# Optimization experiments

Measured on AMD Instinct MI355X. Metric: run time of the kernel, lower is better.

The kernel has to match this reference:

```python
import jax, jax.numpy as jnp
import numpy as np

S = 2048
HIDDEN = 4096
NH, NKV, HD = 32, 8, 128
QPK = NH // NKV  # 4
BLOCK, LOCAL, VERT = 64, 16, 8
ROPE_BASE = 1.0e6
SCALE = 1.0 / HD  # mup scaling: head_dim / mup_attn_multiplier(=1.0)


def setup_inputs() -> dict:
    key = jax.random.key(0)
    ks = jax.random.split(key, 5)
    qkv_out = NKV * (QPK + 2) * HD  # 6144, head-major layout
    return {
        "positions": jnp.arange(S, dtype=jnp.int32),
        "hidden_states": jax.random.normal(ks[0], (S, HIDDEN), jnp.float32),
        "w_qkv": jax.random.normal(ks[1], (qkv_out, HIDDEN), jnp.float32) * 0.02,
        "b_qkv": jax.random.normal(ks[2], (qkv_out,), jnp.float32) * 0.02,
        "w_dense": jax.random.normal(ks[3], (HIDDEN, HIDDEN), jnp.float32) * 0.02,
        "b_dense": jax.random.normal(ks[4], (HIDDEN,), jnp.float32) * 0.02,
    }


def _rope(x, cos, sin):
    # NeoX-style (non-interleaved) rotary over full head_dim.
    # x: [S, n_heads, HD]; cos/sin: [S, HD//2]
    d2 = x.shape[-1] // 2
    x1, x2 = x[..., :d2], x[..., d2:]
    c, s = cos[:, None, :], sin[:, None, :]
    return jnp.concatenate([x1 * c - x2 * s, x2 * c + x1 * s], axis=-1)


def _blocksparse_mask(positions):
    # vllm phi3small pattern: block (qb,kb) active iff causal AND
    # (qb-kb < local_blocks OR (kb + head + 1) % vert_stride == 0), hetero heads.
    qb = positions // BLOCK                       # [S]
    heads = jnp.arange(NH, dtype=positions.dtype)
    diff = qb[:, None] - qb[None, :]              # [S,S]
    local = diff < LOCAL                          # [S,S]
    vert = ((qb[None, None, :] + heads[:, None, None] + 1) % VERT) == 0  # [NH,1,S]
    causal = positions[:, None] >= positions[None, :]                     # [S,S]
    return (local[None] | vert) & causal[None]    # [NH,S,S]


def reference(positions, hidden_states, w_qkv, b_qkv, w_dense, b_dense):
    seq = hidden_states.shape[0]
    qkv = hidden_states @ w_qkv.T + b_qkv                   # [S, 6144]
    qkv = qkv.reshape(seq, NKV, QPK + 2, HD)                # head-major split
    q = qkv[:, :, :QPK].reshape(seq, NH, HD)
    k = qkv[:, :, QPK]                                      # [S, NKV, HD]
    v = qkv[:, :, QPK + 1]

    pos = positions.astype(jnp.float32)  # rope_position_scale = 1.0
    inv_freq = 1.0 / (ROPE_BASE ** (jnp.arange(0, HD, 2, dtype=jnp.float32) / HD))
    freqs = pos[:, None] * inv_freq                          # [S, HD/2]
    cos, sin = jnp.cos(freqs), jnp.sin(freqs)
    q = _rope(q, cos, sin)
    k = _rope(k, cos, sin)

    # GQA: each kv head serves QPK query heads
    kx = jnp.repeat(k, QPK, axis=1)                          # [S, NH, HD]
    vx = jnp.repeat(v, QPK, axis=1)

    scores = jnp.einsum('qhd,khd->hqk', q, kx) * SCALE       # [NH,S,S]
    mask = _blocksparse_mask(positions)
    scores = jnp.where(mask, scores, -jnp.inf)  # diag always in local block -> no empty rows
    p = jax.nn.softmax(scores, axis=-1)
    out = jnp.einsum('hqk,khd->qhd', p, vx).reshape(seq, NH * HD)
    return out @ w_dense.T + b_dense
```

## Files before the change

kernel.cpp:

```cpp
#include <hip/hip_runtime.h>

#define S_LEN   2048
#define HID     4096
#define NHEADS  32
#define NKVH    8
#define HDIM    128
#define NQKV    6144
#define ATT_SCALE (1.0f/128.0f)

typedef unsigned short u16;
typedef __attribute__((ext_vector_type(8))) __bf16 bf16x8;
typedef __attribute__((ext_vector_type(4))) float  f32x4;

__device__ __forceinline__ u16 f2bf(float f) {
    union { float f; unsigned u; } x; x.f = f;
    unsigned u = x.u;
    u += 0x7fffu + ((u >> 16) & 1u);
    return (u16)(u >> 16);
}
__device__ __forceinline__ float bf2f(u16 v) {
    union { unsigned u; float f; } x; x.u = ((unsigned)v) << 16; return x.f;
}

__global__ __launch_bounds__(256) void cvt_bf16_kernel(const float* __restrict__ in,
                                                       u16* __restrict__ out, int n4) {
    int stride = gridDim.x * blockDim.x;
    for (int i = blockIdx.x * blockDim.x + threadIdx.x; i < n4; i += stride) {
        float4 v = *(const float4*)(in + (size_t)i * 4);
        ushort4 o = make_ushort4(f2bf(v.x), f2bf(v.y), f2bf(v.z), f2bf(v.w));
        *(ushort4*)(out + (size_t)i * 4) = o;
    }
}

#define BM 128
#define BN 128
#define BK 32

template <bool OUT_BF16>
__global__ __launch_bounds__(256) void gemm_bt_kernel(
    const u16* __restrict__ A,
    const u16* __restrict__ B,
    const float* __restrict__ bias,
    void* __restrict__ Cout,
    int M, int N, int K)
{
    __shared__ u16 Alds[2][BM][BK];
    __shared__ u16 Blds[2][BN][BK];

    const int tid  = threadIdx.x;
    const int wid  = tid >> 6;
    const int lane = tid & 63;
    const int ln   = lane & 15;
    const int quad = lane >> 4;
    const int wm   = (wid >> 1) * 64;
    const int wn   = (wid & 1) * 64;
    const int tileM = blockIdx.y * BM;
    const int tileN = blockIdx.x * BN;

    const int srow = lane >> 2;
    const int scol = ((lane & 3) ^ ((srow >> 1) & 3)) * 8;

    f32x4 acc[4][4];
    #pragma unroll
    for (int i = 0; i < 4; i++)
        #pragma unroll
        for (int j = 0; j < 4; j++) {
            f32x4 z = {0.f, 0.f, 0.f, 0.f};
            acc[i][j] = z;
        }

    auto stage = [&](int k, int buf) {
        const int k0 = k * BK;
        #pragma unroll
        for (int p = 0; p < 2; p++) {
            int r = p * 64 + wid * 16;
            const u16* ga = A + (size_t)(tileM + r + srow) * K + k0 + scol;
            const u16* gb = B + (size_t)(tileN + r + srow) * K + k0 + scol;
            __builtin_amdgcn_global_load_lds(
                (const __attribute__((address_space(1))) void*)ga,
                (__attribute__((address_space(3))) void*)&Alds[buf][r][0], 16, 0, 0);
            __builtin_amdgcn_global_load_lds(
                (const __attribute__((address_space(1))) void*)gb,
                (__attribute__((address_space(3))) void*)&Blds[buf][r][0], 16, 0, 0);
        }
    };

    const int nIter = K / BK;
    stage(0, 0);

    const int pc = (quad ^ ((ln >> 1) & 3)) * 8;

    for (int k = 0; k < nIter; k++) {
        const int buf = k & 1;
        __syncthreads();
        if (k + 1 < nIter) stage(k + 1, buf ^ 1);

        bf16x8 af[4], bfr[4];
        #pragma unroll
        for (int i = 0; i < 4; i++)
            af[i] = *(const bf16x8*)(&Alds[buf][wm + i * 16 + ln][pc]);
        #pragma unroll
        for (int j = 0; j < 4; j++)
            bfr[j] = *(const bf16x8*)(&Blds[buf][wn + j * 16 + ln][pc]);
        #pragma unroll
        for (int i = 0; i < 4; i++)
            #pragma unroll
            for (int j = 0; j < 4; j++)
                acc[i][j] = __builtin_amdgcn_mfma_f32_16x16x32_bf16(af[i], bfr[j], acc[i][j], 0, 0, 0);
    }

    #pragma unroll
    for (int i = 0; i < 4; i++) {
        #pragma unroll
        for (int j = 0; j < 4; j++) {
            int n = tileN + wn + j * 16 + ln;
            float bv = bias[n];
            #pragma unroll
            for (int r = 0; r < 4; r++) {
                int m = tileM + wm + i * 16 + quad * 4 + r;
                float v = acc[i][j][r] + bv;
                if (OUT_BF16)
                    ((u16*)Cout)[(size_t)m * N + n] = f2bf(v);
                else
                    ((float*)Cout)[(size_t)m * N + n] = v;
            }
        }
    }
}

#define TBM 256
#define TBN 256
#define TBK 64

#define GFENCE() asm volatile("" ::: "memory")
#define GSBAR()  do { GFENCE(); __builtin_amdgcn_s_barrier(); GFENCE(); } while (0)

template <bool OUT_BF16>
__global__ __launch_bounds__(512, 2) void gemm_bt8_kernel(
    const u16* __restrict__ A,
    const u16* __restrict__ B,
    const float* __restrict__ bias,
    void* __restrict__ Cout,
    int M, int N, int K)
{
    __shared__ u16 lds[65536];

    const int tid  = threadIdx.x;
    const int wid  = tid >> 6;
    const int lane = tid & 63;
    const int ln   = lane & 15;
    const int quad = lane >> 4;
    const int wr   = wid >> 2;
    const int wc   = wid & 3;
    const int tileM = blockIdx.y * TBM;
    const int tileN = blockIdx.x * TBN;

    f32x4 acc[2][2][4][2];
    #pragma unroll
    for (int a = 0; a < 2; a++)
        #pragma unroll
        for (int b = 0; b < 2; b++)
            #pragma unroll
            for (int m = 0; m < 4; m++)
                #pragma unroll
                for (int n = 0; n < 2; n++) {
                    f32x4 z = {0.f, 0.f, 0.f, 0.f};
                    acc[a][b][m][n] = z;
                }

    const int srho = lane >> 3;
    const int scol = (((lane & 7) ^ srho) << 3);

    auto stage_half = [&](const u16* Mp, int tbase, int h, int kk, int bb, int isB) {
        const int ldsbase = isB * 32768 + (bb * 2 + h) * 8192;
        #pragma unroll
        for (int s = 0; s < 2; s++) {
            const int rho0 = s * 64 + wid * 8;
            const int rho  = rho0 + srho;
            const u16* src = Mp + (size_t)(tbase + h * 128 + rho) * K + (size_t)kk * TBK + scol;
            __builtin_amdgcn_global_load_lds(
                (const __attribute__((address_space(1))) void*)src,
                (__attribute__((address_space(3))) void*)&lds[ldsbase + rho0 * 64], 16, 0, 0);
        }
    };

    bf16x8 af[4][2];

#define READ_A(a_)                                                                  \
    do {                                                                            \
        _Pragma("unroll")                                                           \
        for (int m = 0; m < 4; m++) {                                               \
            const int ra = wr * 64 + m * 16 + ln;                                   \
            const int ab = (buf * 2 + (a_)) * 8192 + ra * 64;                       \
            const int rx = ra & 7;                                                  \
            af[m][0] = *(const bf16x8*)(&lds[ab + ((quad ^ rx) << 3)]);             \
            af[m][1] = *(const bf16x8*)(&lds[ab + (((4 + quad) ^ rx) << 3)]);       \
        }                                                                           \
    } while (0)

#define READ_B(b_, bfr_)                                                            \
    do {                                                                            \
        _Pragma("unroll")                                                           \
        for (int n = 0; n < 2; n++) {                                               \
            const int rb = wc * 32 + n * 16 + ln;                                   \
            const int bbase = 32768 + (buf * 2 + (b_)) * 8192 + rb * 64;            \
            const int rx = rb & 7;                                                  \
            bfr_[n][0] = *(const bf16x8*)(&lds[bbase + ((quad ^ rx) << 3)]);        \
            bfr_[n][1] = *(const bf16x8*)(&lds[bbase + (((4 + quad) ^ rx) << 3)]);  \
        }                                                                           \
    } while (0)

#define DO_MFMA(a_, b_, bfr_)                                                       \
    do {                                                                            \
        __builtin_amdgcn_s_setprio(1);                                              \
        _Pragma("unroll")                                                           \
        for (int m = 0; m < 4; m++)                                                 \
            _Pragma("unroll")                                                       \
            for (int n = 0; n < 2; n++) {                                           \
                acc[a_][b_][m][n] = __builtin_amdgcn_mfma_f32_16x16x32_bf16(        \
                    af[m][0], bfr_[n][0], acc[a_][b_][m][n], 0, 0, 0);              \
                acc[a_][b_][m][n] = __builtin_amdgcn_mfma_f32_16x16x32_bf16(        \
                    af[m][1], bfr_[n][1], acc[a_][b_][m][n], 0, 0, 0);              \
            }                                                                       \
        __builtin_amdgcn_s_setprio(0);                                              \
    } while (0)

    const int nIter = K / TBK;

    stage_half(A, tileM, 0, 0, 0, 0);
    stage_half(B, tileN, 0, 0, 0, 1);
    stage_half(A, tileM, 1, 0, 0, 0);
    stage_half(B, tileN, 1, 0, 0, 1);

    for (int t = 0; t < nIter; t++) {
        const int buf = t & 1;
        const int bn  = buf ^ 1;
        const int kn  = (t + 1 == nIter) ? 0 : t + 1;

        stage_half(A, tileM, 0, kn, bn, 0);
        asm volatile("s_waitcnt vmcnt(6)" ::: "memory");
        GSBAR();
        {
            bf16x8 bfr[2][2];
            READ_A(0); READ_B(0, bfr);
            DO_MFMA(0, 0, bfr);
            GSBAR();

            stage_half(B, tileN, 0, kn, bn, 1);
            asm volatile("s_waitcnt vmcnt(4)" ::: "memory");
            GSBAR();
            READ_A(1);
            DO_MFMA(1, 0, bfr);
            GSBAR();
        }

        stage_half(A, tileM, 1, kn, bn, 0);
        GSBAR();
        {
            bf16x8 bfr[2][2];
            READ_B(1, bfr);
            DO_MFMA(1, 1, bfr);
            GSBAR();

            stage_half(B, tileN, 1, kn, bn, 1);
            GSBAR();
            READ_A(0);
            DO_MFMA(0, 1, bfr);
            GSBAR();
        }
    }

    asm volatile("s_waitcnt vmcnt(0)" ::: "memory");

#undef READ_A
#undef READ_B
#undef DO_MFMA

    #pragma unroll
    for (int a = 0; a < 2; a++)
        #pragma unroll
        for (int b = 0; b < 2; b++)
            #pragma unroll
            for (int n = 0; n < 2; n++) {
                #pragma unroll
                for (int m = 0; m < 4; m++) {
                    const int col = tileN + b * 128 + wc * 32 + n * 16 + ln;
                    const float bv = bias[col];
                    #pragma unroll
                    for (int r = 0; r < 4; r++) {
                        const int row = tileM + a * 128 + wr * 64 + m * 16 + quad * 4 + r;
                        float v = acc[a][b][m][n][r] + bv;
                        if (OUT_BF16)
                            ((u16*)Cout)[(size_t)row * N + col] = f2bf(v);
                        else
                            ((float*)Cout)[(size_t)row * N + col] = v;
                    }
                }
            }
}

__global__ __launch_bounds__(128) void rope_split_kernel(
    const u16* __restrict__ qkv, const int* __restrict__ positions,
    u16* __restrict__ qb_o, u16* __restrict__ kb_o, u16* __restrict__ vb_o)
{
    const int d   = threadIdx.x;
    const int pos = blockIdx.x;
    const int hy  = blockIdx.y;
    const float p = (float)positions[pos];

    if (hy >= NHEADS + NKVH) {
        int kv = hy - NHEADS - NKVH;
        const u16* src = qkv + (size_t)pos * NQKV + (kv * 6 + 5) * HDIM;
        vb_o[((size_t)kv * S_LEN + pos) * HDIM + d] = src[d];
        return;
    }
    const u16* src;
    u16* dst;
    if (hy < NHEADS) {
        int kv = hy >> 2, qi = hy & 3;
        src = qkv + (size_t)pos * NQKV + (kv * 6 + qi) * HDIM;
        dst = qb_o + ((size_t)hy * S_LEN + pos) * HDIM;
    } else {
        int kv = hy - NHEADS;
        src = qkv + (size_t)pos * NQKV + (kv * 6 + 4) * HDIM;
        dst = kb_o + ((size_t)kv * S_LEN + pos) * HDIM;
    }
    int d2 = d & 63;
    float inv = expf(-(float)d2 * (13.815510557964274f / 64.0f));
    float fr = p * inv;
    float s, c;
    sincosf(fr, &s, &c);
    float x1 = bf2f(src[d2]);
    float x2 = bf2f(src[d2 + 64]);
    float o = (d < 64) ? (x1 * c - x2 * s) : (x2 * c + x1 * s);
    dst[d] = f2bf(o);
}

__global__ __launch_bounds__(256, 4) void attn_bs_kernel(
    const u16* __restrict__ Q,
    const u16* __restrict__ K,
    const u16* __restrict__ V,
    u16* __restrict__ O)
{
    __shared__ u16 Ks[64 * 128];
    __shared__ u16 Vt[128 * 64];
    __shared__ u16 Ps[4][16 * 64];

    const int qb = (int)gridDim.x - 1 - (int)blockIdx.x;
    const int h  = blockIdx.y;
    const int kv = h >> 2;
    const int tid  = threadIdx.x;
    const int w    = tid >> 6;
    const int lane = tid & 63;
    const int ln   = lane & 15;
    const int quad = lane >> 4;

    bf16x8 aq[4];
    {
        const u16* Qg = Q + ((size_t)h * S_LEN + qb * 64 + w * 16 + ln) * HDIM + quad * 8;
        #pragma unroll
        for (int ks = 0; ks < 4; ks++)
            aq[ks] = *(const bf16x8*)(Qg + ks * 32);
    }

    f32x4 oacc[8];
    #pragma unroll
    for (int n = 0; n < 8; n++) { f32x4 z = {0.f,0.f,0.f,0.f}; oacc[n] = z; }
    float mrow[4] = {-1e30f, -1e30f, -1e30f, -1e30f};
    float lrow[4] = {0.f, 0.f, 0.f, 0.f};

    for (int kb = 0; kb <= qb; kb++) {
        bool sel = (qb - kb < 16) || (((kb + h + 1) & 7) == 0);
        if (!sel) continue;

        __syncthreads();

        const u16* Kg = K + ((size_t)kv * S_LEN + kb * 64) * HDIM;
        const u16* Vg = V + ((size_t)kv * S_LEN + kb * 64) * HDIM;

        #pragma unroll
        for (int p = 0; p < 4; p++) {
            int r0  = w * 16 + p * 4;
            int row = r0 + (lane >> 4);
            const u16* src = Kg + (size_t)row * HDIM + (((lane & 15) ^ (row & 7)) << 3);
            __builtin_amdgcn_global_load_lds(
                (const __attribute__((address_space(1))) void*)src,
                (__attribute__((address_space(3))) void*)&Ks[r0 * 128], 16, 0, 0);
        }

        {
            int dbase = w * 32;
            #pragma unroll
            for (int p = 0; p < 4; p++) {
                int d0 = dbase + p * 8;
                uint4 vv = *(const uint4*)(Vg + (size_t)lane * HDIM + d0);
                const u16* pvv = (const u16*)&vv;
                #pragma unroll
                for (int jj = 0; jj < 8; jj++) {
                    int d = d0 + jj;
                    Vt[d * 64 + ((((lane >> 3)) ^ (d & 7)) << 3) + (lane & 7)] = pvv[jj];
                }
            }
        }
        __syncthreads();

        f32x4 sacc[4];
        #pragma unroll
        for (int jj = 0; jj < 4; jj++) { f32x4 z = {0.f,0.f,0.f,0.f}; sacc[jj] = z; }
        __builtin_amdgcn_s_setprio(1);
        #pragma unroll
        for (int ks = 0; ks < 4; ks++) {
            #pragma unroll
            for (int jj = 0; jj < 4; jj++) {
                bf16x8 bk = *(const bf16x8*)(
                    &Ks[(jj * 16 + ln) * 128 + (((ks * 4 + quad) ^ (ln & 7)) << 3)]);
                sacc[jj] = __builtin_amdgcn_mfma_f32_16x16x32_bf16(aq[ks], bk, sacc[jj], 0, 0, 0);
            }
        }
        __builtin_amdgcn_s_setprio(0);

        #pragma unroll
        for (int r = 0; r < 4; r++) {
            float pv[4];
            float mx = -1e30f;
            const int qrow = w * 16 + quad * 4 + r;
            #pragma unroll
            for (int jj = 0; jj < 4; jj++) {
                float s = sacc[jj][r] * ATT_SCALE;
                if (kb == qb && (jj * 16 + ln) > qrow) s = -1e30f;
                pv[jj] = s;
                mx = fmaxf(mx, s);
            }
            #pragma unroll
            for (int off = 1; off < 16; off <<= 1)
                mx = fmaxf(mx, __shfl_xor(mx, off, 64));
            float mnew  = fmaxf(mrow[r], mx);
            float alpha = __expf(mrow[r] - mnew);
            float sum = 0.f;
            #pragma unroll
            for (int jj = 0; jj < 4; jj++) {
                float pe = __expf(pv[jj] - mnew);
                pv[jj] = pe;
                sum += pe;
            }
            #pragma unroll
            for (int off = 1; off < 16; off <<= 1)
                sum += __shfl_xor(sum, off, 64);
            lrow[r] = lrow[r] * alpha + sum;
            mrow[r] = mnew;
            #pragma unroll
            for (int n = 0; n < 8; n++) oacc[n][r] *= alpha;
            const int prow = quad * 4 + r;
            #pragma unroll
            for (int jj = 0; jj < 4; jj++)
                Ps[w][prow * 64 + (((jj * 2 + (ln >> 3)) ^ (prow & 7)) << 3) + (ln & 7)]
                    = f2bf(pv[jj]);
        }

        __builtin_amdgcn_s_setprio(1);
        #pragma unroll
        for (int kk = 0; kk < 2; kk++) {
            bf16x8 ap = *(const bf16x8*)(
                &Ps[w][ln * 64 + (((kk * 4 + quad) ^ (ln & 7)) << 3)]);
            #pragma unroll
            for (int n = 0; n < 8; n++) {
                bf16x8 bv = *(const bf16x8*)(
                    &Vt[(n * 16 + ln) * 64 + (((kk * 4 + quad) ^ (ln & 7)) << 3)]);
                oacc[n] = __builtin_amdgcn_mfma_f32_16x16x32_bf16(ap, bv, oacc[n], 0, 0, 0);
            }
        }
        __builtin_amdgcn_s_setprio(0);
    }

    #pragma unroll
    for (int n = 0; n < 8; n++) {
        #pragma unroll
        for (int r = 0; r < 4; r++) {
            int row = w * 16 + quad * 4 + r;
            int pos = qb * 64 + row;
            float o = oacc[n][r] / lrow[r];
            O[(size_t)pos * (NHEADS * HDIM) + h * HDIM + n * 16 + ln] = f2bf(o);
        }
    }
}

extern "C" void kernel_launch(void* const* d_in, const int* in_sizes, int n_in,
                              void* d_out, int out_size, void* d_ws, size_t ws_size,
                              hipStream_t stream) {
    const int*   positions = (const int*)d_in[0];
    const float* hidden    = (const float*)d_in[1];
    const float* w_qkv     = (const float*)d_in[2];
    const float* b_qkv     = (const float*)d_in[3];
    const float* w_dense   = (const float*)d_in[4];
    const float* b_dense   = (const float*)d_in[5];
    float* out = (float*)d_out;

    char* ws = (char*)d_ws;
    u16* ws_h    = (u16*)(ws);
    u16* ws_wqkv = (u16*)(ws + 16777216);
    u16* ws_wd   = (u16*)(ws + 67108864);
    u16* ws_qkv  = (u16*)(ws + 100663296);
    u16* ws_q    = (u16*)(ws + 125829120);
    u16* ws_k    = (u16*)(ws + 142606336);
    u16* ws_v    = (u16*)(ws + 146800640);
    u16* ws_attn = (u16*)(ws + 150994944);

    cvt_bf16_kernel<<<1024, 256, 0, stream>>>(hidden,  ws_h,    (S_LEN * HID) / 4);
    cvt_bf16_kernel<<<2048, 256, 0, stream>>>(w_qkv,   ws_wqkv, (NQKV * HID) / 4);
    cvt_bf16_kernel<<<2048, 256, 0, stream>>>(w_dense, ws_wd,   (HID * HID) / 4);

    gemm_bt8_kernel<true><<<dim3(NQKV / TBN, S_LEN / TBM), 512, 0, stream>>>(
        ws_h, ws_wqkv, b_qkv, ws_qkv, S_LEN, NQKV, HID);

    rope_split_kernel<<<dim3(S_LEN, NHEADS + 2 * NKVH), 128, 0, stream>>>(
        ws_qkv, positions, ws_q, ws_k, ws_v);

    attn_bs_kernel<<<dim3(S_LEN / 64, NHEADS), 256, 0, stream>>>(ws_q, ws_k, ws_v, ws_attn);

    gemm_bt_kernel<false><<<dim3(HID / BN, S_LEN / BM), 256, 0, stream>>>(
        ws_attn, ws_wd, b_dense, out, S_LEN, HID, HID);
}
```

Baseline: 562.5 us.

## Hold both A and B fragment halves in registers to cut GEMM barriers

The GEMM main loop now loads both A halves and both B halves into separate register fragments. It then issues all four MFMA quadrants with fewer workgroup barriers per K-step, reusing the fragments instead of re-reading A from LDS. Fewer barriers and LDS reads should let global-to-LDS staging overlap more with MFMA work. The cost is extra VGPR pressure, plus a need to check that the LDS writes into the next buffer cannot race with reads still in flight.

```diff
diff --git a/kernel.cpp b/kernel.cpp
--- a/kernel.cpp
+++ b/kernel.cpp
@@ -184,17 +184,15 @@
         }
     };
 
-    bf16x8 af[4][2];
-
-#define READ_A(a_)                                                                  \
+#define READ_A(a_, af_)                                                             \
     do {                                                                            \
         _Pragma("unroll")                                                           \
         for (int m = 0; m < 4; m++) {                                               \
             const int ra = wr * 64 + m * 16 + ln;                                   \
             const int ab = (buf * 2 + (a_)) * 8192 + ra * 64;                       \
             const int rx = ra & 7;                                                  \
-            af[m][0] = *(const bf16x8*)(&lds[ab + ((quad ^ rx) << 3)]);             \
-            af[m][1] = *(const bf16x8*)(&lds[ab + (((4 + quad) ^ rx) << 3)]);       \
+            af_[m][0] = *(const bf16x8*)(&lds[ab + ((quad ^ rx) << 3)]);            \
+            af_[m][1] = *(const bf16x8*)(&lds[ab + (((4 + quad) ^ rx) << 3)]);      \
         }                                                                           \
     } while (0)
 
@@ -210,7 +208,7 @@
         }                                                                           \
     } while (0)
 
-#define DO_MFMA(a_, b_, bfr_)                                                       \
+#define DO_MFMA(a_, b_, af_, bfr_)                                                  \
     do {                                                                            \
         __builtin_amdgcn_s_setprio(1);                                              \
         _Pragma("unroll")                                                           \
@@ -218,9 +216,9 @@
             _Pragma("unroll")                                                       \
             for (int n = 0; n < 2; n++) {                                           \
                 acc[a_][b_][m][n] = __builtin_amdgcn_mfma_f32_16x16x32_bf16(        \
-                    af[m][0], bfr_[n][0], acc[a_][b_][m][n], 0, 0, 0);              \
+                    af_[m][0], bfr_[n][0], acc[a_][b_][m][n], 0, 0, 0);             \
                 acc[a_][b_][m][n] = __builtin_amdgcn_mfma_f32_16x16x32_bf16(        \
-                    af[m][1], bfr_[n][1], acc[a_][b_][m][n], 0, 0, 0);              \
+                    af_[m][1], bfr_[n][1], acc[a_][b_][m][n], 0, 0, 0);             \
             }                                                                       \
         __builtin_amdgcn_s_setprio(0);                                              \
     } while (0)
@@ -232,6 +230,8 @@
     stage_half(A, tileM, 1, 0, 0, 0);
     stage_half(B, tileN, 1, 0, 0, 1);
 
+    bf16x8 af0[4][2], af1[4][2], bfr0[2][2], bfr1[2][2];
+
     for (int t = 0; t < nIter; t++) {
         const int buf = t & 1;
         const int bn  = buf ^ 1;
@@ -240,34 +240,23 @@
         stage_half(A, tileM, 0, kn, bn, 0);
         asm volatile("s_waitcnt vmcnt(6)" ::: "memory");
         GSBAR();
-        {
-            bf16x8 bfr[2][2];
-            READ_A(0); READ_B(0, bfr);
-            DO_MFMA(0, 0, bfr);
-            GSBAR();
-
-            stage_half(B, tileN, 0, kn, bn, 1);
-            asm volatile("s_waitcnt vmcnt(4)" ::: "memory");
-            GSBAR();
-            READ_A(1);
-            DO_MFMA(1, 0, bfr);
-            GSBAR();
-        }
+        READ_A(0, af0); READ_B(0, bfr0);
+        DO_MFMA(0, 0, af0, bfr0);
+
+        stage_half(B, tileN, 0, kn, bn, 1);
+        asm volatile("s_waitcnt vmcnt(4)" ::: "memory");
+        GSBAR();
+        READ_A(1, af1); READ_B(1, bfr1);
+        DO_MFMA(1, 0, af1, bfr0);
 
         stage_half(A, tileM, 1, kn, bn, 0);
+        DO_MFMA(1, 1, af1, bfr1);
+
+        stage_half(B, tileN, 1, kn, bn, 1);
+        DO_MFMA(0, 1, af0, bfr1);
+
+        asm volatile("s_waitcnt lgkmcnt(0)" ::: "memory");
         GSBAR();
-        {
-            bf16x8 bfr[2][2];
-            READ_B(1, bfr);
-            DO_MFMA(1, 1, bfr);
-            GSBAR();
-
-            stage_half(B, tileN, 1, kn, bn, 1);
-            GSBAR();
-            READ_A(0);
-            DO_MFMA(0, 1, bfr);
-            GSBAR();
-        }
     }
 
     asm volatile("s_waitcnt vmcnt(0)" ::: "memory");
```

New measurement: 553.6 us. About the same (-1.6%).
